# Optimization experiments

Hardware: AMD Instinct MI355X
Metric: run time of the kernel (lower is better)

## Reference

```python
import jax, jax.numpy as jnp
import numpy as np

B, S, D = 4, 2048, 1024
H, HD = 16, 64
WINDOW = 256


def setup_inputs() -> dict:
    key = jax.random.key(0)
    ks = jax.random.split(key, 5)
    scale = 1.0 / np.sqrt(D)
    return {
        "hidden_states": jax.random.normal(ks[0], (B, S, D), dtype=jnp.float32),
        "Wq": jax.random.normal(ks[1], (D, D), dtype=jnp.float32) * scale,
        "Wk": jax.random.normal(ks[2], (D, D), dtype=jnp.float32) * scale,
        "Wv": jax.random.normal(ks[3], (D, D), dtype=jnp.float32) * scale,
        "Wo": jax.random.normal(ks[4], (D, D), dtype=jnp.float32) * scale,
        "bo": jnp.zeros((D,), dtype=jnp.float32),
    }


def reference(hidden_states, Wq, Wk, Wv, Wo, bo):
    # q/k/v projections (no bias), torch Linear: x @ W.T
    q = hidden_states @ Wq.T  # [B,S,D]
    k = hidden_states @ Wk.T
    v = hidden_states @ Wv.T

    def split_heads(t):  # [B,S,D] -> [B,H,S,HD]
        return t.reshape(B, S, H, HD).transpose(0, 2, 1, 3)

    q, k, v = split_heads(q), split_heads(k), split_heads(v)

    # NOTE: original code does NOT scale by 1/sqrt(head_dim)
    scores = jnp.einsum("bhqd,bhkd->bhqk", q.astype(jnp.float32), k.astype(jnp.float32))

    # local causal band mask: keep j <= i and i - j < WINDOW
    i = jnp.arange(S)[:, None]
    j = jnp.arange(S)[None, :]
    band = (j <= i) & (i - j < WINDOW)  # [S,S] bool
    mask_value = jnp.finfo(scores.dtype).min
    scores = jnp.where(band[None, None, :, :], scores, mask_value)

    attn = jax.nn.softmax(scores, axis=-1).astype(v.dtype)
    ctx = jnp.einsum("bhqk,bhkd->bhqd", attn, v)  # [B,H,S,HD]

    # merge heads -> [B,S,D]
    ctx = ctx.transpose(0, 2, 1, 3).reshape(B, S, D)
    out = ctx @ Wo.T + bo
    return out
```

## Files before the change

### kernel.cpp

```cpp
#include <hip/hip_runtime.h>
#include <hip/hip_bf16.h>
#include <cstdint>
#include <cstddef>

#define S_LEN   2048
#define BATCH   4
#define NHEAD   16
#define HDIM    64
#define DMODEL  1024
#define WIN     256
#define PQ      72

typedef __bf16 bf16x8 __attribute__((ext_vector_type(8)));
typedef float f32x4 __attribute__((ext_vector_type(4)));
typedef unsigned short u16x4 __attribute__((ext_vector_type(4)));
typedef unsigned short u16x8 __attribute__((ext_vector_type(8)));

__device__ __forceinline__ unsigned short f2bf(float x) {
  union { float f; unsigned u; } c; c.f = x;
  unsigned r = (c.u + 0x7fffu + ((c.u >> 16) & 1u)) >> 16;
  return (unsigned short)r;
}

__device__ __forceinline__ void gld_lds16(const void* g, void* l) {
  __builtin_amdgcn_global_load_lds(
      (__attribute__((address_space(1))) void*)g,
      (__attribute__((address_space(3))) void*)l, 16, 0, 0);
}

__global__ __launch_bounds__(256) void convert_kernel(
    const float* __restrict__ s0, const float* __restrict__ s1,
    const float* __restrict__ s2, const float* __restrict__ s3,
    const float* __restrict__ s4,
    unsigned short* __restrict__ d0, unsigned short* __restrict__ d1,
    unsigned short* __restrict__ d2, unsigned short* __restrict__ d3,
    unsigned short* __restrict__ d4) {
  const int z = blockIdx.y;
  const float* s; unsigned short* d; long n;
  if      (z == 0) { s = s0; d = d0; n = (long)8192 * 1024; }
  else if (z == 1) { s = s1; d = d1; n = (long)1024 * 1024; }
  else if (z == 2) { s = s2; d = d2; n = (long)1024 * 1024; }
  else if (z == 3) { s = s3; d = d3; n = (long)1024 * 1024; }
  else             { s = s4; d = d4; n = (long)1024 * 1024; }
  const long base = ((long)blockIdx.x * 256 + threadIdx.x) * 16;
  if (base >= n) return;
#pragma unroll
  for (int i = 0; i < 4; ++i) {
    const float4 f = *(const float4*)(s + base + i * 4);
    u16x4 ov;
    ov.x = f2bf(f.x); ov.y = f2bf(f.y); ov.z = f2bf(f.z); ov.w = f2bf(f.w);
    *(u16x4*)(d + base + i * 4) = ov;
  }
}

template <int MODE>
__device__ __forceinline__ void gemm_bt_core(
    const unsigned short* __restrict__ A, const unsigned short* __restrict__ B,
    void* __restrict__ C, const float* __restrict__ bias,
    int M, int N, int K) {
  const int m0 = blockIdx.x * 128;
  const int n0 = blockIdx.y * 128;
  const int tid  = threadIdx.x;
  const int wave = tid >> 6, lane = tid & 63;
  const int quad = lane >> 4, l16 = lane & 15;
  const int wm = wave >> 1, wn = wave & 1;

  __shared__ unsigned short lsA[128 * 64];
  __shared__ unsigned short lsB[128 * 64];

  f32x4 acc[4][4];
#pragma unroll
  for (int i = 0; i < 4; ++i)
#pragma unroll
    for (int j = 0; j < 4; ++j) acc[i][j] = f32x4{0.f, 0.f, 0.f, 0.f};

  const int trow   = tid >> 3;
  const int tchunk = tid & 7;
  const int swz_w  = (trow >> 1) & 7;
  const int scol   = ((tchunk ^ swz_w) << 3);
  const int swz_r  = (l16 >> 1) & 7;

  for (int k0 = 0; k0 < K; k0 += 64) {
    __syncthreads();
#pragma unroll
    for (int c = 0; c < 4; ++c) {
      const int row  = trow + 32 * c;
      const int flat = row * 64 + tchunk * 8;
      gld_lds16(A + (size_t)(m0 + row) * K + k0 + scol, lsA + flat);
      gld_lds16(B + (size_t)(n0 + row) * K + k0 + scol, lsB + flat);
    }
    __syncthreads();

#pragma unroll
    for (int s2 = 0; s2 < 2; ++s2) {
      bf16x8 af[4], bfr[4];
#pragma unroll
      for (int mi = 0; mi < 4; ++mi)
        af[mi] = *(const bf16x8*)(lsA + (wm * 64 + mi * 16 + l16) * 64 +
                                  (((s2 * 4 + quad) ^ swz_r) << 3));
#pragma unroll
      for (int ni = 0; ni < 4; ++ni)
        bfr[ni] = *(const bf16x8*)(lsB + (wn * 64 + ni * 16 + l16) * 64 +
                                   (((s2 * 4 + quad) ^ swz_r) << 3));
#pragma unroll
      for (int mi = 0; mi < 4; ++mi)
#pragma unroll
        for (int ni = 0; ni < 4; ++ni)
          acc[mi][ni] = __builtin_amdgcn_mfma_f32_16x16x32_bf16(
              af[mi], bfr[ni], acc[mi][ni], 0, 0, 0);
    }
  }

#pragma unroll
  for (int mi = 0; mi < 4; ++mi) {
#pragma unroll
    for (int r = 0; r < 4; ++r) {
      const int m = m0 + wm * 64 + mi * 16 + quad * 4 + r;
#pragma unroll
      for (int ni = 0; ni < 4; ++ni) {
        const int n = n0 + wn * 64 + ni * 16 + l16;
        const float vv = acc[mi][ni][r];
        if (MODE == 0) {
          ((unsigned short*)C)[(size_t)m * N + n] = f2bf(vv);
        } else {
          ((float*)C)[(size_t)m * N + n] = vv + bias[n];
        }
      }
    }
  }
}

__global__ __launch_bounds__(256) void gemm_proj_kernel(
    const unsigned short* __restrict__ A, const unsigned short* __restrict__ B,
    unsigned short* __restrict__ C, int M, int N, int K) {
  gemm_bt_core<0>(A, B, C, nullptr, M, N, K);
}

__global__ __launch_bounds__(256) void gemm_out_kernel(
    const unsigned short* __restrict__ A, const unsigned short* __restrict__ B,
    float* __restrict__ C, const float* __restrict__ bias, int M, int N, int K) {
  gemm_bt_core<1>(A, B, C, bias, M, N, K);
}

__global__ __launch_bounds__(256) void transpose_v_kernel(
    const unsigned short* __restrict__ v, unsigned short* __restrict__ vt) {
  const int bh = blockIdx.y;
  const int b = bh >> 4, h = bh & 15;
  const int s0 = blockIdx.x * 64;
  __shared__ unsigned short t[64][PQ];
  const int r = threadIdx.x >> 2, cb = (threadIdx.x & 3) * 16;
  const unsigned short* src =
      v + ((size_t)(b * S_LEN + s0 + r) * DMODEL + h * HDIM + cb);
  *(u16x8*)(&t[r][cb])     = *(const u16x8*)src;
  *(u16x8*)(&t[r][cb + 8]) = *(const u16x8*)(src + 8);
  __syncthreads();
  const int d = threadIdx.x >> 2, sc = (threadIdx.x & 3) * 16;
  u16x8 o0, o1;
#pragma unroll
  for (int jj = 0; jj < 8; ++jj) { o0[jj] = t[sc + jj][d]; o1[jj] = t[sc + 8 + jj][d]; }
  unsigned short* dst = vt + ((size_t)(bh * HDIM + d) * S_LEN + s0 + sc);
  *(u16x8*)dst       = o0;
  *(u16x8*)(dst + 8) = o1;
}

__global__ __launch_bounds__(256) void attn_kernel(
    const unsigned short* __restrict__ q, const unsigned short* __restrict__ k,
    const unsigned short* __restrict__ vt, unsigned short* __restrict__ ctx) {
  const int bh = blockIdx.y;
  const int b = bh >> 4, h = bh & 15;
  const int i0 = blockIdx.x * 128;
  const int tid  = threadIdx.x;
  const int wave = tid >> 6, lane = tid & 63;
  const int quad = lane >> 4, l16 = lane & 15;

  __shared__ unsigned short lsQ[128 * PQ];
  __shared__ unsigned short lsK[64 * PQ];
  __shared__ unsigned short lsVp[64 * PQ];

  {
    const int r = tid >> 1, cb = (tid & 1) * 32;
    const unsigned short* src =
        q + ((size_t)(b * S_LEN + i0 + r) * DMODEL + h * HDIM + cb);
    *(u16x8*)(lsQ + r * PQ + cb)      = *(const u16x8*)src;
    *(u16x8*)(lsQ + r * PQ + cb + 8)  = *(const u16x8*)(src + 8);
    *(u16x8*)(lsQ + r * PQ + cb + 16) = *(const u16x8*)(src + 16);
    *(u16x8*)(lsQ + r * PQ + cb + 24) = *(const u16x8*)(src + 24);
  }
  __syncthreads();

  bf16x8 aq[2][2];
#pragma unroll
  for (int t = 0; t < 2; ++t)
#pragma unroll
    for (int s2 = 0; s2 < 2; ++s2)
      aq[t][s2] = *(const bf16x8*)(lsQ + (wave * 32 + t * 16 + l16) * PQ +
                                   s2 * 32 + quad * 8);

  float l_lane[2] = {0.f, 0.f};
  f32x4 o[2][4];
#pragma unroll
  for (int t = 0; t < 2; ++t)
#pragma unroll
    for (int nd = 0; nd < 4; ++nd) o[t][nd] = f32x4{0.f, 0.f, 0.f, 0.f};

  const int jb0 = (i0 >= WIN) ? ((i0 - WIN + 1) >> 6) : 0;
  const int jb1 = (i0 + 127) >> 6;
  const int jbi = i0 >> 6;

  for (int jb = jb0; jb <= jb1; ++jb) {
    const int j0 = jb * 64;
    const bool needMask = !(jb == jbi - 1 || jb == jbi - 2);
    __syncthreads();
    {
      const int r = tid >> 2, cb = (tid & 3) * 16;
      const unsigned short* ks =
          k + ((size_t)(b * S_LEN + j0 + r) * DMODEL + h * HDIM + cb);
      *(u16x8*)(lsK + r * PQ + cb)     = *(const u16x8*)ks;
      *(u16x8*)(lsK + r * PQ + cb + 8) = *(const u16x8*)(ks + 8);
      const unsigned short* vs =
          vt + ((size_t)(bh * HDIM + r) * S_LEN + j0 + cb);
      const u16x8 va = *(const u16x8*)vs;
      const u16x8 vb = *(const u16x8*)(vs + 8);
      const int jhi = cb >> 4;
      const int base = (jhi >> 1) * 32 + (jhi & 1) * 4;
      u16x4 w0, w1, w2, w3;
      w0[0]=va[0];  w0[1]=va[1];  w0[2]=va[2];  w0[3]=va[3];
      w1[0]=va[4];  w1[1]=va[5];  w1[2]=va[6];  w1[3]=va[7];
      w2[0]=vb[0];  w2[1]=vb[1];  w2[2]=vb[2];  w2[3]=vb[3];
      w3[0]=vb[4];  w3[1]=vb[5];  w3[2]=vb[6];  w3[3]=vb[7];
      *(u16x4*)(lsVp + r * PQ + base)      = w0;
      *(u16x4*)(lsVp + r * PQ + base + 8)  = w1;
      *(u16x4*)(lsVp + r * PQ + base + 16) = w2;
      *(u16x4*)(lsVp + r * PQ + base + 24) = w3;
    }
    __syncthreads();

    f32x4 st[2][4];
#pragma unroll
    for (int t = 0; t < 2; ++t)
#pragma unroll
      for (int ni = 0; ni < 4; ++ni) st[t][ni] = f32x4{0.f, 0.f, 0.f, 0.f};
#pragma unroll
    for (int s2 = 0; s2 < 2; ++s2) {
      bf16x8 bk[4];
#pragma unroll
      for (int ni = 0; ni < 4; ++ni)
        bk[ni] = *(const bf16x8*)(lsK + (ni * 16 + l16) * PQ + s2 * 32 + quad * 8);
#pragma unroll
      for (int t = 0; t < 2; ++t)
#pragma unroll
        for (int ni = 0; ni < 4; ++ni)
          st[t][ni] = __builtin_amdgcn_mfma_f32_16x16x32_bf16(
              bk[ni], aq[t][s2], st[t][ni], 0, 0, 0);
    }

    bf16x8 ap[2][2];
#pragma unroll
    for (int t = 0; t < 2; ++t) {
      const int iq = i0 + wave * 32 + t * 16 + l16;
      if (needMask) {
#pragma unroll
        for (int ni = 0; ni < 4; ++ni)
#pragma unroll
          for (int r = 0; r < 4; ++r) {
            const int j = j0 + ni * 16 + quad * 4 + r;
            const bool ok = (j <= iq) && (iq - j < WIN);
            const float p = ok ? __expf(fminf(st[t][ni][r], 80.f)) : 0.f;
            st[t][ni][r] = p;
            l_lane[t] += p;
          }
      } else {
#pragma unroll
        for (int ni = 0; ni < 4; ++ni)
#pragma unroll
          for (int r = 0; r < 4; ++r) {
            const float p = __expf(fminf(st[t][ni][r], 80.f));
            st[t][ni][r] = p;
            l_lane[t] += p;
          }
      }
#pragma unroll
      for (int s2 = 0; s2 < 2; ++s2) {
        bf16x8 a;
#pragma unroll
        for (int r = 0; r < 4; ++r) {
          union { unsigned short u; __bf16 h; } c0, c1;
          c0.u = f2bf(st[t][2 * s2][r]);
          c1.u = f2bf(st[t][2 * s2 + 1][r]);
          a[r]     = c0.h;
          a[4 + r] = c1.h;
        }
        ap[t][s2] = a;
      }
    }

#pragma unroll
    for (int s2 = 0; s2 < 2; ++s2) {
      bf16x8 bv[4];
#pragma unroll
      for (int nd = 0; nd < 4; ++nd)
        bv[nd] = *(const bf16x8*)(lsVp + (nd * 16 + l16) * PQ + s2 * 32 + quad * 8);
#pragma unroll
      for (int t = 0; t < 2; ++t)
#pragma unroll
        for (int nd = 0; nd < 4; ++nd)
          o[t][nd] = __builtin_amdgcn_mfma_f32_16x16x32_bf16(
              ap[t][s2], bv[nd], o[t][nd], 0, 0, 0);
    }
  }

#pragma unroll
  for (int t = 0; t < 2; ++t) {
    float l = l_lane[t];
    l += __shfl_xor(l, 16, 64);
    l += __shfl_xor(l, 32, 64);
    const float invl = 1.f / l;
#pragma unroll
    for (int r = 0; r < 4; ++r) {
      const float inv = __shfl(invl, quad * 4 + r, 64);
      const int i = i0 + wave * 32 + t * 16 + quad * 4 + r;
#pragma unroll
      for (int nd = 0; nd < 4; ++nd)
        ctx[(size_t)(b * S_LEN + i) * DMODEL + h * HDIM + nd * 16 + l16] =
            f2bf(o[t][nd][r] * inv);
    }
  }
}

extern "C" void kernel_launch(void* const* d_in, const int* in_sizes, int n_in,
                              void* d_out, int out_size, void* d_ws, size_t ws_size,
                              hipStream_t stream) {
  const float* hs = (const float*)d_in[0];
  const float* Wq = (const float*)d_in[1];
  const float* Wk = (const float*)d_in[2];
  const float* Wv = (const float*)d_in[3];
  const float* Wo = (const float*)d_in[4];
  const float* bo = (const float*)d_in[5];
  float* out = (float*)d_out;

  const size_t MD = (size_t)8192 * 1024;
  const size_t DD = (size_t)1024 * 1024;
  unsigned short* hsb  = (unsigned short*)d_ws;
  unsigned short* wqb  = hsb + MD;
  unsigned short* wkb  = wqb + DD;
  unsigned short* wvb  = wkb + DD;
  unsigned short* wob  = wvb + DD;
  unsigned short* qb   = wob + DD;
  unsigned short* kb   = qb + MD;
  unsigned short* vb   = kb + MD;
  unsigned short* ctxb = vb + MD;
  unsigned short* vtb  = ctxb + MD;

  convert_kernel<<<dim3(2048, 5), 256, 0, stream>>>(hs, Wq, Wk, Wv, Wo,
                                                    hsb, wqb, wkb, wvb, wob);
  gemm_proj_kernel<<<dim3(64, 8), 256, 0, stream>>>(hsb, wqb, qb, 8192, 1024, 1024);
  gemm_proj_kernel<<<dim3(64, 8), 256, 0, stream>>>(hsb, wkb, kb, 8192, 1024, 1024);
  gemm_proj_kernel<<<dim3(64, 8), 256, 0, stream>>>(hsb, wvb, vb, 8192, 1024, 1024);
  transpose_v_kernel<<<dim3(32, 64), 256, 0, stream>>>(vb, vtb);
  attn_kernel<<<dim3(16, 64), 256, 0, stream>>>(qb, kb, vtb, ctxb);
  gemm_out_kernel<<<dim3(64, 8), 256, 0, stream>>>(ctxb, wob, out, bo,
                                                   8192, 1024, 1024);
}
```

Baseline: 233.3 us.

## Merge QKV projections into one launch and write V transposed in epilogue

```diff
diff --git a/kernel.cpp b/kernel.cpp
--- a/kernel.cpp
+++ b/kernel.cpp
@@ -113,54 +113,56 @@
 
 #pragma unroll
   for (int mi = 0; mi < 4; ++mi) {
-#pragma unroll
-    for (int r = 0; r < 4; ++r) {
-      const int m = m0 + wm * 64 + mi * 16 + quad * 4 + r;
+    if (MODE == 2) {
+      const int mB = m0 + wm * 64 + mi * 16 + quad * 4;
+      const int bq = mB >> 11, s = mB & 2047;
 #pragma unroll
       for (int ni = 0; ni < 4; ++ni) {
         const int n = n0 + wn * 64 + ni * 16 + l16;
-        const float vv = acc[mi][ni][r];
-        if (MODE == 0) {
-          ((unsigned short*)C)[(size_t)m * N + n] = f2bf(vv);
-        } else {
-          ((float*)C)[(size_t)m * N + n] = vv + bias[n];
+        u16x4 w;
+        w[0] = f2bf(acc[mi][ni][0]); w[1] = f2bf(acc[mi][ni][1]);
+        w[2] = f2bf(acc[mi][ni][2]); w[3] = f2bf(acc[mi][ni][3]);
+        *(u16x4*)((unsigned short*)C +
+                  (((size_t)((bq << 4) | (n >> 6)) * 64 + (n & 63)) << 11) + s) = w;
+      }
+    } else {
+#pragma unroll
+      for (int r = 0; r < 4; ++r) {
+        const int m = m0 + wm * 64 + mi * 16 + quad * 4 + r;
+#pragma unroll
+        for (int ni = 0; ni < 4; ++ni) {
+          const int n = n0 + wn * 64 + ni * 16 + l16;
+          const float vv = acc[mi][ni][r];
+          if (MODE == 0) {
+            ((unsigned short*)C)[(size_t)m * N + n] = f2bf(vv);
+          } else {
+            ((float*)C)[(size_t)m * N + n] = vv + bias[n];
+          }
         }
       }
     }
   }
 }
 
-__global__ __launch_bounds__(256) void gemm_proj_kernel(
-    const unsigned short* __restrict__ A, const unsigned short* __restrict__ B,
-    unsigned short* __restrict__ C, int M, int N, int K) {
-  gemm_bt_core<0>(A, B, C, nullptr, M, N, K);
+__global__ __launch_bounds__(256) void gemm_qkv_kernel(
+    const unsigned short* __restrict__ A,
+    const unsigned short* __restrict__ B0, const unsigned short* __restrict__ B1,
+    const unsigned short* __restrict__ B2,
+    unsigned short* __restrict__ C0, unsigned short* __restrict__ C1,
+    unsigned short* __restrict__ Cv, int M, int N, int K) {
+  if (blockIdx.z == 2) {
+    gemm_bt_core<2>(A, B2, Cv, nullptr, M, N, K);
+  } else {
+    const unsigned short* B = blockIdx.z == 0 ? B0 : B1;
+    unsigned short*       C = blockIdx.z == 0 ? C0 : C1;
+    gemm_bt_core<0>(A, B, C, nullptr, M, N, K);
+  }
 }
 
 __global__ __launch_bounds__(256) void gemm_out_kernel(
     const unsigned short* __restrict__ A, const unsigned short* __restrict__ B,
     float* __restrict__ C, const float* __restrict__ bias, int M, int N, int K) {
   gemm_bt_core<1>(A, B, C, bias, M, N, K);
-}
-
-__global__ __launch_bounds__(256) void transpose_v_kernel(
-    const unsigned short* __restrict__ v, unsigned short* __restrict__ vt) {
-  const int bh = blockIdx.y;
-  const int b = bh >> 4, h = bh & 15;
-  const int s0 = blockIdx.x * 64;
-  __shared__ unsigned short t[64][PQ];
-  const int r = threadIdx.x >> 2, cb = (threadIdx.x & 3) * 16;
-  const unsigned short* src =
-      v + ((size_t)(b * S_LEN + s0 + r) * DMODEL + h * HDIM + cb);
-  *(u16x8*)(&t[r][cb])     = *(const u16x8*)src;
-  *(u16x8*)(&t[r][cb + 8]) = *(const u16x8*)(src + 8);
-  __syncthreads();
-  const int d = threadIdx.x >> 2, sc = (threadIdx.x & 3) * 16;
-  u16x8 o0, o1;
-#pragma unroll
-  for (int jj = 0; jj < 8; ++jj) { o0[jj] = t[sc + jj][d]; o1[jj] = t[sc + 8 + jj][d]; }
-  unsigned short* dst = vt + ((size_t)(bh * HDIM + d) * S_LEN + s0 + sc);
-  *(u16x8*)dst       = o0;
-  *(u16x8*)(dst + 8) = o1;
 }
 
 __global__ __launch_bounds__(256) void attn_kernel(
@@ -347,16 +349,13 @@
   unsigned short* wob  = wvb + DD;
   unsigned short* qb   = wob + DD;
   unsigned short* kb   = qb + MD;
-  unsigned short* vb   = kb + MD;
-  unsigned short* ctxb = vb + MD;
-  unsigned short* vtb  = ctxb + MD;
+  unsigned short* vtb  = kb + MD;
+  unsigned short* ctxb = vtb + MD;
 
   convert_kernel<<<dim3(2048, 5), 256, 0, stream>>>(hs, Wq, Wk, Wv, Wo,
                                                     hsb, wqb, wkb, wvb, wob);
-  gemm_proj_kernel<<<dim3(64, 8), 256, 0, stream>>>(hsb, wqb, qb, 8192, 1024, 1024);
-  gemm_proj_kernel<<<dim3(64, 8), 256, 0, stream>>>(hsb, wkb, kb, 8192, 1024, 1024);
-  gemm_proj_kernel<<<dim3(64, 8), 256, 0, stream>>>(hsb, wvb, vb, 8192, 1024, 1024);
-  transpose_v_kernel<<<dim3(32, 64), 256, 0, stream>>>(vb, vtb);
+  gemm_qkv_kernel<<<dim3(64, 8, 3), 256, 0, stream>>>(hsb, wqb, wkb, wvb,
+                                                      qb, kb, vtb, 8192, 1024, 1024);
   attn_kernel<<<dim3(16, 64), 256, 0, stream>>>(qb, kb, vtb, ctxb);
   gemm_out_kernel<<<dim3(64, 8), 256, 0, stream>>>(ctxb, wob, out, bo,
                                                    8192, 1024, 1024);
```

Result: faster. 220.7 us (-5.4%).
